# Kernel optimization log

Hardware: AMD Instinct MI355X
Metric: run time of the kernel (lower is better)

The kernel has to match this reference:

```python
import jax, jax.numpy as jnp
import numpy as np

LOG2PI = float(np.log(2.0 * np.pi))


def setup_inputs() -> dict:
    key = jax.random.key(0)
    ks = jax.random.split(key, 5)
    B, T, XD, C = 128, 2050, 6, 64
    return {
        "x": jax.random.normal(ks[0], (B, T, XD), jnp.float32),
        "observation_means": jax.random.uniform(ks[1], (C, XD), dtype=jnp.float32),
        "observation_stddevs": jax.random.uniform(ks[2], (C, XD), dtype=jnp.float32),
        "log_A": jax.random.normal(ks[3], (C, C), jnp.float32),
        "log_pi": jax.random.normal(ks[4], (C,), jnp.float32),
    }


def _emission_logprob(x, means, stds):
    # Normal(means[:, :4], relu(stds[:, :4]) + 0.1).log_prob(x[:, :, :4]) summed over feat dim
    mu = means[:, :4]                       # (C,4)
    sigma = jax.nn.relu(stds[:, :4]) + 0.1  # (C,4)
    z = (x[:, :, None, :4] - mu) / sigma    # (B,T,C,4)
    return jnp.sum(-0.5 * z * z - jnp.log(sigma) - 0.5 * LOG2PI, axis=-1)  # (B,T,C)


def _forward_scalers(logp, log_A, log_pi):
    # scaled HMM forward pass; returns per-step log normalizers (T,B)
    a0 = logp[:, 0] + log_pi
    s0 = jax.nn.logsumexp(a0, axis=-1)
    a0n = a0 - s0[:, None]

    def step(a_prev, lp_t):
        a = lp_t + jax.nn.logsumexp(a_prev[:, :, None] + log_A[None], axis=1)
        s = jax.nn.logsumexp(a, axis=-1)
        return a - s[:, None], s

    _, s_rest = jax.lax.scan(step, a0n, jnp.swapaxes(logp[:, 1:], 0, 1))
    return jnp.concatenate([s0[None], s_rest], axis=0)  # (T,B)


def _viterbi(logp, log_A, log_pi):
    d0 = logp[:, 0] + log_pi  # (B,C)

    def step(d_prev, lp_t):
        scores = d_prev[:, :, None] + log_A[None]  # (B,C_prev,C_cur)
        psi_t = jnp.argmax(scores, axis=1)
        d = jnp.max(scores, axis=1) + lp_t
        return d, psi_t

    d_last, psi = jax.lax.scan(step, d0, jnp.swapaxes(logp[:, 1:], 0, 1))  # psi: (T-1,B,C)
    c_last = jnp.argmax(d_last, axis=-1)  # (B,)

    def back(c_next, psi_t):
        c_t = jnp.take_along_axis(psi_t, c_next[:, None], axis=1)[:, 0]
        return c_t, c_t

    _, cs = jax.lax.scan(back, c_last, psi, reverse=True)  # (T-1,B)
    c = jnp.concatenate([cs, c_last[None]], axis=0)  # (T,B)
    return jnp.swapaxes(c, 0, 1)  # (B,T)


def reference(x, observation_means, observation_stddevs, log_A, log_pi):
    logA = jax.nn.log_softmax(log_A, axis=1)
    logpi = jax.nn.log_softmax(log_pi, axis=0)
    logp = _emission_logprob(x, observation_means, observation_stddevs)  # (B,T,C)
    scalers = _forward_scalers(logp, logA, logpi)                         # (T,B)
    logp_x = jnp.sum(scalers, axis=0)                                     # (B,)
    c_est = _viterbi(logp, logA, logpi)                                   # (B,T) int
    return logp_x, c_est
```

## Files before the change

kernel.cpp:

```cpp
#include <hip/hip_runtime.h>

#define T_LEN 2050
#define B_SZ 128
#define NCHUNK 33
#define HL2PI 0.91893853320467274178f

__device__ __forceinline__ float waveMax(float v) {
#pragma unroll
    for (int off = 32; off >= 1; off >>= 1)
        v = fmaxf(v, __shfl_xor(v, off, 64));
    return v;
}
__device__ __forceinline__ float waveSum(float v) {
#pragma unroll
    for (int off = 32; off >= 1; off >>= 1)
        v += __shfl_xor(v, off, 64);
    return v;
}
__device__ __forceinline__ void waveArgmax(float& v, int& idx) {
#pragma unroll
    for (int off = 32; off >= 1; off >>= 1) {
        float ov = __shfl_xor(v, off, 64);
        int   oi = __shfl_xor(idx, off, 64);
        if (ov > v || (ov == v && oi < idx)) { v = ov; idx = oi; }
    }
}
__device__ __forceinline__ void cfence() { asm volatile("" ::: "memory"); }

__device__ __forceinline__ float dppSumAll(float v) {
#define SSTEP(ctrl) { int t_ = __builtin_amdgcn_update_dpp(0, __float_as_int(v), ctrl, 0xf, 0xf, true); \
                      v = v + __int_as_float(t_); }
    SSTEP(0x111) SSTEP(0x112) SSTEP(0x114) SSTEP(0x118) SSTEP(0x142) SSTEP(0x143)
#undef SSTEP
    return __int_as_float(__builtin_amdgcn_readlane(__float_as_int(v), 63));
}
__device__ __forceinline__ float dppMaxAll(float v) {
#define MSTEP(ctrl) { int t_ = __builtin_amdgcn_update_dpp(__float_as_int(v), __float_as_int(v), ctrl, 0xf, 0xf, false); \
                      v = fmaxf(v, __int_as_float(t_)); }
    MSTEP(0x111) MSTEP(0x112) MSTEP(0x114) MSTEP(0x118) MSTEP(0x142) MSTEP(0x143)
#undef MSTEP
    return __int_as_float(__builtin_amdgcn_readlane(__float_as_int(v), 63));
}

extern "C" __global__ __launch_bounds__(64, 1)
void hmm_prep(const float* __restrict__ logA_in,
              const float* __restrict__ logpi_in,
              float* __restrict__ lAg,
              float* __restrict__ lpig)
{
    __shared__ float la[64 * 65];
    __shared__ float rowlse[64];
    const int j = threadIdx.x;
#pragma unroll
    for (int k = 0; k < 64; ++k)
        la[k * 65 + j] = logA_in[k * 64 + j];
    cfence();
    {
        float m = -1e30f;
#pragma unroll
        for (int k = 0; k < 64; ++k) m = fmaxf(m, la[j * 65 + k]);
        float s = 0.f;
#pragma unroll
        for (int k = 0; k < 64; ++k) s += expf(la[j * 65 + k] - m);
        rowlse[j] = m + logf(s);
    }
    cfence();
    {
        float v = logpi_in[j];
        float m = waveMax(v);
        float s = waveSum(expf(v - m));
        lpig[j] = v - (m + logf(s));
    }
    float4* o = (float4*)lAg;
#pragma unroll
    for (int k = 0; k < 16; ++k) {
        float4 v;
        v.x = la[(4 * k + 0) * 65 + j] - rowlse[4 * k + 0];
        v.y = la[(4 * k + 1) * 65 + j] - rowlse[4 * k + 1];
        v.z = la[(4 * k + 2) * 65 + j] - rowlse[4 * k + 2];
        v.w = la[(4 * k + 3) * 65 + j] - rowlse[4 * k + 3];
        o[j * 16 + k] = v;
    }
}

extern "C" __global__ __launch_bounds__(256)
void hmm_emis(const float* __restrict__ x,
              const float* __restrict__ means,
              const float* __restrict__ stds,
              float* __restrict__ buf,
              float* __restrict__ m_pre)
{
    const int wid = blockIdx.x * 4 + (threadIdx.x >> 6);
    const int j = threadIdx.x & 63;
    const int t = wid >> 7;
    const int b = wid & 127;

    const float* xt = x + ((size_t)b * T_LEN + t) * 6;
    float x0 = xt[0], x1 = xt[1], x2 = xt[2], x3 = xt[3];

    float mu0 = means[j * 6 + 0], mu1 = means[j * 6 + 1];
    float mu2 = means[j * 6 + 2], mu3 = means[j * 6 + 3];
    float sg0 = fmaxf(stds[j * 6 + 0], 0.f) + 0.1f;
    float sg1 = fmaxf(stds[j * 6 + 1], 0.f) + 0.1f;
    float sg2 = fmaxf(stds[j * 6 + 2], 0.f) + 0.1f;
    float sg3 = fmaxf(stds[j * 6 + 3], 0.f) + 0.1f;
    float ls0 = logf(sg0), ls1 = logf(sg1), ls2 = logf(sg2), ls3 = logf(sg3);

    float z0 = (x0 - mu0) / sg0, z1 = (x1 - mu1) / sg1;
    float z2 = (x2 - mu2) / sg2, z3 = (x3 - mu3) / sg3;
    float e0 = ((-0.5f * z0) * z0 - ls0) - HL2PI;
    float e1 = ((-0.5f * z1) * z1 - ls1) - HL2PI;
    float e2 = ((-0.5f * z2) * z2 - ls2) - HL2PI;
    float e3 = ((-0.5f * z3) * z3 - ls3) - HL2PI;
    float lp = ((e0 + e1) + e2) + e3;

    buf[((size_t)b * T_LEN + t) * 64 + j] = lp;
    float mm = waveMax(lp);
    if (j == 0) m_pre[(size_t)b * T_LEN + t] = mm;
}

extern "C" __global__ __launch_bounds__(64, 1)
void hmm_main(const float* __restrict__ x,
              const float* __restrict__ means,
              const float* __restrict__ stds,
              const float* __restrict__ lAg,
              const float* __restrict__ lpig,
              float* __restrict__ out,
              float* __restrict__ buf,
              const float* __restrict__ m_pre,
              int* __restrict__ c_last)
{
    __shared__ __align__(16) float xs[12304];
    __shared__ __align__(16) float pbuf[64];

    const int j   = threadIdx.x;
    const int bid = blockIdx.x;
    const bool is_fwd = (bid < B_SZ);
    const int b = is_fwd ? bid : bid - B_SZ;

    float lpi = lpig[j];
    const float4* pv = (const float4*)pbuf;

    if (is_fwd) {
        {
            const float4* xg4 = (const float4*)(x + (size_t)b * T_LEN * 6);
            float4* xs4 = (float4*)xs;
            for (int i = j; i < 3075; i += 64) xs4[i] = xg4[i];
        }
        float mu0 = means[j * 6 + 0], mu1 = means[j * 6 + 1];
        float mu2 = means[j * 6 + 2], mu3 = means[j * 6 + 3];
        float sg0 = fmaxf(stds[j * 6 + 0], 0.f) + 0.1f;
        float sg1 = fmaxf(stds[j * 6 + 1], 0.f) + 0.1f;
        float sg2 = fmaxf(stds[j * 6 + 2], 0.f) + 0.1f;
        float sg3 = fmaxf(stds[j * 6 + 3], 0.f) + 0.1f;
        float ls0 = logf(sg0), ls1 = logf(sg1), ls2 = logf(sg2), ls3 = logf(sg3);
        float i0 = 1.f / sg0, i1 = 1.f / sg1, i2 = 1.f / sg2, i3 = 1.f / sg3;
        float cst = -(ls0 + ls1 + ls2 + ls3) - 4.f * HL2PI;

        float Ac[64];
        {
            const float4* g = (const float4*)lAg;
#pragma unroll
            for (int k = 0; k < 16; ++k) {
                float4 v = g[j * 16 + k];
                Ac[4 * k + 0] = __expf(v.x); Ac[4 * k + 1] = __expf(v.y);
                Ac[4 * k + 2] = __expf(v.z); Ac[4 * k + 3] = __expf(v.w);
            }
        }
        cfence();

        float z0 = (xs[0] - mu0) * i0, z1 = (xs[1] - mu1) * i1;
        float z2 = (xs[2] - mu2) * i2, z3 = (xs[3] - mu3) * i3;
        float a0 = (cst - 0.5f * (z0 * z0 + z1 * z1 + z2 * z2 + z3 * z3)) + lpi;
        float m0a = dppMaxAll(a0);
        float u = __expf(a0 - m0a);
        float s0 = dppSumAll(u);
        double acc = (double)(m0a + __logf(s0));
        u *= (1.0f / s0);
        pbuf[j] = u;
        float4 rr[16];
#pragma unroll
        for (int k = 0; k < 16; ++k) rr[k] = pv[k];

        const float* mp = m_pre + (size_t)b * T_LEN;
        float g0 = mp[1], g1 = mp[2], g2 = mp[3], g3 = mp[4];

#pragma unroll 1
        for (int t = 1; t < T_LEN; ++t) {
            float mm_c = g0; g0 = g1; g1 = g2; g2 = g3;
            int tp = t + 4; if (tp > T_LEN - 1) tp = T_LEN - 1;
            g3 = mp[tp];

            int o = t * 6;
            float y0 = xs[o], y1 = xs[o + 1], y2 = xs[o + 2], y3 = xs[o + 3];
            float w0 = (y0 - mu0) * i0, w1 = (y1 - mu1) * i1;
            float w2 = (y2 - mu2) * i2, w3 = (y3 - mu3) * i3;
            float lp = cst - 0.5f * (w0 * w0 + w1 * w1 + w2 * w2 + w3 * w3);
            float e_c = __expf(lp - mm_c);

            float q0 = 0.f, q1 = 0.f, q2 = 0.f, q3 = 0.f;
#pragma unroll
            for (int k = 0; k < 16; ++k) {
                float4 pp = rr[k];
                q0 = fmaf(pp.x, Ac[4 * k + 0], q0);
                q1 = fmaf(pp.y, Ac[4 * k + 1], q1);
                q2 = fmaf(pp.z, Ac[4 * k + 2], q2);
                q3 = fmaf(pp.w, Ac[4 * k + 3], q3);
            }
            u = ((q0 + q1) + (q2 + q3)) * e_c;
            acc += (double)mm_c;
            if ((t & 3) == 0) {
                float ss = dppSumAll(u);
                acc += (double)__logf(ss);
                u *= (1.0f / ss);
            }

            pbuf[j] = u;
#pragma unroll
            for (int k = 0; k < 16; ++k) rr[k] = pv[k];
        }
        float sf = dppSumAll(u);
        acc += (double)__logf(sf);
        if (j == 0) out[b] = (float)acc;
    } else {
        float lA[64];
        {
            const float4* g = (const float4*)lAg;
#pragma unroll
            for (int k = 0; k < 16; ++k) {
                float4 v = g[j * 16 + k];
                lA[4 * k + 0] = v.x; lA[4 * k + 1] = v.y;
                lA[4 * k + 2] = v.z; lA[4 * k + 3] = v.w;
            }
        }
        float* bb = buf + (size_t)b * T_LEN * 64 + j;

        float dn = bb[0] + lpi;
        float l0 = bb[64], l1 = bb[128], l2 = bb[192], l3 = bb[256];
        bb[0] = dn;
        pbuf[j] = dn;
        float4 rr[16];
#pragma unroll
        for (int k = 0; k < 16; ++k) rr[k] = pv[k];

#pragma unroll 1
        for (int t = 1; t < T_LEN; ++t) {
            float lp_c = l0; l0 = l1; l1 = l2; l2 = l3;
            int tp = t + 4; if (tp > T_LEN - 1) tp = T_LEN - 1;
            l3 = bb[(size_t)tp * 64];

            float m0 = -3.4e38f, m1 = -3.4e38f, m2 = -3.4e38f, m3 = -3.4e38f;
#pragma unroll
            for (int k = 0; k < 16; ++k) {
                float4 dd = rr[k];
                m0 = fmaxf(m0, dd.x + lA[4 * k + 0]);
                m1 = fmaxf(m1, dd.y + lA[4 * k + 1]);
                m2 = fmaxf(m2, dd.z + lA[4 * k + 2]);
                m3 = fmaxf(m3, dd.w + lA[4 * k + 3]);
            }
            dn = fmaxf(fmaxf(m0, m1), fmaxf(m2, m3)) + lp_c;

            bb[(size_t)t * 64] = dn;
            pbuf[j] = dn;
#pragma unroll
            for (int k = 0; k < 16; ++k) rr[k] = pv[k];
        }

        float vv = dn; int idx = j;
        waveArgmax(vv, idx);
        if (j == 0) c_last[b] = idx;
    }
}

extern "C" __global__ __launch_bounds__(256)
void hmm_psi(const float* __restrict__ buf,
             const float* __restrict__ lAg,
             unsigned char* __restrict__ psi)
{
    __shared__ __align__(16) float sd[4][64];
    const int warp = threadIdx.x >> 6;
    const int j = threadIdx.x & 63;
    const int wid = blockIdx.x * 4 + warp;

    float lA[64];
    {
        const float4* g = (const float4*)lAg;
#pragma unroll
        for (int k = 0; k < 16; ++k) {
            float4 v = g[j * 16 + k];
            lA[4 * k + 0] = v.x; lA[4 * k + 1] = v.y;
            lA[4 * k + 2] = v.z; lA[4 * k + 3] = v.w;
        }
    }
    const float4* dv = (const float4*)sd[warp];
    const int NP = 2049 * B_SZ;

    for (int p = wid; p < NP; p += 8192) {
        const int t = (p >> 7) + 1;
        const int b = p & 127;
        float dval = buf[((size_t)b * T_LEN + (t - 1)) * 64 + j];
        sd[warp][j] = dval;

        float bv0 = -3.4e38f, bv1 = -3.4e38f, bv2 = -3.4e38f, bv3 = -3.4e38f;
        int bi0 = 0, bi1 = 1, bi2 = 2, bi3 = 3;
#pragma unroll
        for (int k = 0; k < 16; ++k) {
            float4 dd = dv[k];
            float v0 = dd.x + lA[4 * k + 0];
            float v1 = dd.y + lA[4 * k + 1];
            float v2 = dd.z + lA[4 * k + 2];
            float v3 = dd.w + lA[4 * k + 3];
            if (v0 > bv0) { bv0 = v0; bi0 = 4 * k + 0; }
            if (v1 > bv1) { bv1 = v1; bi1 = 4 * k + 1; }
            if (v2 > bv2) { bv2 = v2; bi2 = 4 * k + 2; }
            if (v3 > bv3) { bv3 = v3; bi3 = 4 * k + 3; }
        }
        float best = bv0; int bidx = bi0;
        if (bv1 > best || (bv1 == best && bi1 < bidx)) { best = bv1; bidx = bi1; }
        if (bv2 > best || (bv2 == best && bi2 < bidx)) { best = bv2; bidx = bi2; }
        if (bv3 > best || (bv3 == best && bi3 < bidx)) { best = bv3; bidx = bi3; }

        psi[((size_t)t * B_SZ + b) * 64 + j] = (unsigned char)bidx;
    }
}

extern "C" __global__ __launch_bounds__(256)
void hmm_compose(const unsigned char* __restrict__ psi,
                 unsigned char* __restrict__ mt)
{
    const int w = blockIdx.x * 4 + (threadIdx.x >> 6);
    const int j = threadIdx.x & 63;
    const int g = w % NCHUNK;
    const int b = w / NCHUNK;
    const int e = (g < NCHUNK - 1) ? g * 64 + 64 : (T_LEN - 1);
    int M = j;
    for (int t = e; t >= g * 64 + 1; --t)
        M = psi[((size_t)t * B_SZ + b) * 64 + M];
    mt[((size_t)g * B_SZ + b) * 64 + j] = (unsigned char)M;
}

extern "C" __global__ __launch_bounds__(64, 1)
void hmm_fill(const unsigned char* __restrict__ psi,
              const unsigned char* __restrict__ mt,
              const int* __restrict__ c_last,
              float* __restrict__ out)
{
    __shared__ int sb[NCHUNK];
    const int b = blockIdx.x;
    const int g = threadIdx.x;
    const int cl = c_last[b];
    if (g == 0) {
        int cur = cl;
        for (int q = NCHUNK - 1; q >= 0; --q) {
            cur = mt[((size_t)q * B_SZ + b) * 64 + cur];
            sb[q] = cur;
        }
    }
    cfence();
    float* oc = out + B_SZ + (size_t)b * T_LEN;
    if (g == NCHUNK) {
        oc[T_LEN - 1] = (float)cl;
    } else if (g < NCHUNK) {
        const int e = (g < NCHUNK - 1) ? g * 64 + 64 : (T_LEN - 1);
        int s = (g < NCHUNK - 1) ? sb[g + 1] : cl;
        for (int t = e; t >= g * 64 + 1; --t) {
            s = psi[((size_t)t * B_SZ + b) * 64 + s];
            oc[t - 1] = (float)s;
        }
    }
}

extern "C" void kernel_launch(void* const* d_in, const int* in_sizes, int n_in,
                              void* d_out, int out_size, void* d_ws, size_t ws_size,
                              hipStream_t stream)
{
    const float* x      = (const float*)d_in[0];
    const float* means  = (const float*)d_in[1];
    const float* stds   = (const float*)d_in[2];
    const float* logA   = (const float*)d_in[3];
    const float* logpi  = (const float*)d_in[4];
    float* out = (float*)d_out;

    char* base = (char*)d_ws;
    float*         buf   = (float*)base;
    unsigned char* psi   = (unsigned char*)(base + 67174400);
    float*         m_pre = (float*)(base + 67174400);
    unsigned char* mt    = (unsigned char*)(base + 83968000);
    int*           cl    = (int*)(base + 84238336);
    float*         lAg   = (float*)(base + 84238848);
    float*         lpig  = (float*)(base + 84255232);

    hipLaunchKernelGGL(hmm_prep, dim3(1), dim3(64), 0, stream, logA, logpi, lAg, lpig);
    hipLaunchKernelGGL(hmm_emis, dim3((T_LEN * B_SZ) / 4), dim3(256), 0, stream,
                       x, means, stds, buf, m_pre);
    hipLaunchKernelGGL(hmm_main, dim3(2 * B_SZ), dim3(64), 0, stream,
                       x, means, stds, lAg, lpig, out, buf, m_pre, cl);
    hipLaunchKernelGGL(hmm_psi, dim3(2048), dim3(256), 0, stream, buf, lAg, psi);
    hipLaunchKernelGGL(hmm_compose, dim3((NCHUNK * B_SZ) / 4), dim3(256), 0, stream, psi, mt);
    hipLaunchKernelGGL(hmm_fill, dim3(B_SZ), dim3(64), 0, stream, psi, mt, cl, out);
}
```

Baseline: 1.055 ms.

## Split HMM recurrence inner product across two wavefronts per batch

The sequential forward and Viterbi recurrence in hmm_main now uses two wavefronts per block. Each wavefront reduces over half of the 64 previous states, and the partial sums or maxima are combined through shared memory with a block barrier every time step. This halves the per-step FMA and max chain and the register footprint per lane. In exchange it adds a __syncthreads and an LDS round trip to every one of roughly 2050 serial steps, which may cost more than the arithmetic it saves.

```diff
diff --git a/kernel.cpp b/kernel.cpp
--- a/kernel.cpp
+++ b/kernel.cpp
@@ -119,7 +119,7 @@
     if (j == 0) m_pre[(size_t)b * T_LEN + t] = mm;
 }
 
-extern "C" __global__ __launch_bounds__(64, 1)
+extern "C" __global__ __launch_bounds__(128, 1)
 void hmm_main(const float* __restrict__ x,
               const float* __restrict__ means,
               const float* __restrict__ stds,
@@ -131,21 +131,25 @@
               int* __restrict__ c_last)
 {
     __shared__ __align__(16) float xs[12304];
-    __shared__ __align__(16) float pbuf[64];
-
-    const int j   = threadIdx.x;
+    __shared__ __align__(16) float uperm[2][64];
+    __shared__ float pexch[2][2][64];
+
+    const int tid = threadIdx.x;
+    const int w   = tid >> 6;
+    const int j   = tid & 63;
     const int bid = blockIdx.x;
     const bool is_fwd = (bid < B_SZ);
     const int b = is_fwd ? bid : bid - B_SZ;
+    const int slot = (j & 3) * 16 + (j >> 2);
 
     float lpi = lpig[j];
-    const float4* pv = (const float4*)pbuf;
+    const float4* pv = (const float4*)(&uperm[w][32 * w]);
 
     if (is_fwd) {
         {
             const float4* xg4 = (const float4*)(x + (size_t)b * T_LEN * 6);
             float4* xs4 = (float4*)xs;
-            for (int i = j; i < 3075; i += 64) xs4[i] = xg4[i];
+            for (int i = tid; i < 3075; i += 128) xs4[i] = xg4[i];
         }
         float mu0 = means[j * 6 + 0], mu1 = means[j * 6 + 1];
         float mu2 = means[j * 6 + 2], mu3 = means[j * 6 + 3];
@@ -157,17 +161,24 @@
         float i0 = 1.f / sg0, i1 = 1.f / sg1, i2 = 1.f / sg2, i3 = 1.f / sg3;
         float cst = -(ls0 + ls1 + ls2 + ls3) - 4.f * HL2PI;
 
-        float Ac[64];
+        float Aa[16], Ab[16];
         {
             const float4* g = (const float4*)lAg;
-#pragma unroll
-            for (int k = 0; k < 16; ++k) {
-                float4 v = g[j * 16 + k];
-                Ac[4 * k + 0] = __expf(v.x); Ac[4 * k + 1] = __expf(v.y);
-                Ac[4 * k + 2] = __expf(v.z); Ac[4 * k + 3] = __expf(v.w);
+            if (w == 0) {
+#pragma unroll
+                for (int k = 0; k < 16; ++k) {
+                    float4 v = g[j * 16 + k];
+                    Aa[k] = __expf(v.x); Ab[k] = __expf(v.y);
+                }
+            } else {
+#pragma unroll
+                for (int k = 0; k < 16; ++k) {
+                    float4 v = g[j * 16 + k];
+                    Aa[k] = __expf(v.z); Ab[k] = __expf(v.w);
+                }
             }
         }
-        cfence();
+        __syncthreads();
 
         float z0 = (xs[0] - mu0) * i0, z1 = (xs[1] - mu1) * i1;
         float z2 = (xs[2] - mu2) * i2, z3 = (xs[3] - mu3) * i3;
@@ -177,10 +188,10 @@
         float s0 = dppSumAll(u);
         double acc = (double)(m0a + __logf(s0));
         u *= (1.0f / s0);
-        pbuf[j] = u;
-        float4 rr[16];
-#pragma unroll
-        for (int k = 0; k < 16; ++k) rr[k] = pv[k];
+        uperm[w][slot] = u;
+        float4 rrA[8];
+#pragma unroll
+        for (int k = 0; k < 8; ++k) rrA[k] = pv[k];
 
         const float* mp = m_pre + (size_t)b * T_LEN;
         float g0 = mp[1], g1 = mp[2], g2 = mp[3], g3 = mp[4];
@@ -198,16 +209,23 @@
             float lp = cst - 0.5f * (w0 * w0 + w1 * w1 + w2 * w2 + w3 * w3);
             float e_c = __expf(lp - mm_c);
 
-            float q0 = 0.f, q1 = 0.f, q2 = 0.f, q3 = 0.f;
-#pragma unroll
-            for (int k = 0; k < 16; ++k) {
-                float4 pp = rr[k];
-                q0 = fmaf(pp.x, Ac[4 * k + 0], q0);
-                q1 = fmaf(pp.y, Ac[4 * k + 1], q1);
-                q2 = fmaf(pp.z, Ac[4 * k + 2], q2);
-                q3 = fmaf(pp.w, Ac[4 * k + 3], q3);
+            float qa = 0.f, qb = 0.f;
+#pragma unroll
+            for (int c = 0; c < 4; ++c) {
+                float4 va = rrA[c], vb = rrA[4 + c];
+                qa = fmaf(va.x, Aa[4 * c + 0], qa);
+                qa = fmaf(va.y, Aa[4 * c + 1], qa);
+                qa = fmaf(va.z, Aa[4 * c + 2], qa);
+                qa = fmaf(va.w, Aa[4 * c + 3], qa);
+                qb = fmaf(vb.x, Ab[4 * c + 0], qb);
+                qb = fmaf(vb.y, Ab[4 * c + 1], qb);
+                qb = fmaf(vb.z, Ab[4 * c + 2], qb);
+                qb = fmaf(vb.w, Ab[4 * c + 3], qb);
             }
-            u = ((q0 + q1) + (q2 + q3)) * e_c;
+            float part = qa + qb;
+            pexch[t & 1][w][j] = part;
+            __syncthreads();
+            u = (part + pexch[t & 1][w ^ 1][j]) * e_c;
             acc += (double)mm_c;
             if ((t & 3) == 0) {
                 float ss = dppSumAll(u);
@@ -215,33 +233,41 @@
                 u *= (1.0f / ss);
             }
 
-            pbuf[j] = u;
-#pragma unroll
-            for (int k = 0; k < 16; ++k) rr[k] = pv[k];
+            uperm[w][slot] = u;
+#pragma unroll
+            for (int k = 0; k < 8; ++k) rrA[k] = pv[k];
         }
         float sf = dppSumAll(u);
         acc += (double)__logf(sf);
-        if (j == 0) out[b] = (float)acc;
+        if (w == 0 && j == 0) out[b] = (float)acc;
     } else {
-        float lA[64];
+        float Aa[16], Ab[16];
         {
             const float4* g = (const float4*)lAg;
-#pragma unroll
-            for (int k = 0; k < 16; ++k) {
-                float4 v = g[j * 16 + k];
-                lA[4 * k + 0] = v.x; lA[4 * k + 1] = v.y;
-                lA[4 * k + 2] = v.z; lA[4 * k + 3] = v.w;
+            if (w == 0) {
+#pragma unroll
+                for (int k = 0; k < 16; ++k) {
+                    float4 v = g[j * 16 + k];
+                    Aa[k] = v.x; Ab[k] = v.y;
+                }
+            } else {
+#pragma unroll
+                for (int k = 0; k < 16; ++k) {
+                    float4 v = g[j * 16 + k];
+                    Aa[k] = v.z; Ab[k] = v.w;
+                }
             }
         }
         float* bb = buf + (size_t)b * T_LEN * 64 + j;
 
         float dn = bb[0] + lpi;
         float l0 = bb[64], l1 = bb[128], l2 = bb[192], l3 = bb[256];
-        bb[0] = dn;
-        pbuf[j] = dn;
-        float4 rr[16];
-#pragma unroll
-        for (int k = 0; k < 16; ++k) rr[k] = pv[k];
+        __syncthreads();
+        if (w == 0) bb[0] = dn;
+        uperm[w][slot] = dn;
+        float4 rrA[8];
+#pragma unroll
+        for (int k = 0; k < 8; ++k) rrA[k] = pv[k];
 
 #pragma unroll 1
         for (int t = 1; t < T_LEN; ++t) {
@@ -249,26 +275,33 @@
             int tp = t + 4; if (tp > T_LEN - 1) tp = T_LEN - 1;
             l3 = bb[(size_t)tp * 64];
 
-            float m0 = -3.4e38f, m1 = -3.4e38f, m2 = -3.4e38f, m3 = -3.4e38f;
-#pragma unroll
-            for (int k = 0; k < 16; ++k) {
-                float4 dd = rr[k];
-                m0 = fmaxf(m0, dd.x + lA[4 * k + 0]);
-                m1 = fmaxf(m1, dd.y + lA[4 * k + 1]);
-                m2 = fmaxf(m2, dd.z + lA[4 * k + 2]);
-                m3 = fmaxf(m3, dd.w + lA[4 * k + 3]);
+            float ma = -3.4e38f, mb = -3.4e38f;
+#pragma unroll
+            for (int c = 0; c < 4; ++c) {
+                float4 va = rrA[c], vb = rrA[4 + c];
+                float a0_ = va.x + Aa[4 * c + 0], a1_ = va.y + Aa[4 * c + 1];
+                float a2_ = va.z + Aa[4 * c + 2], a3_ = va.w + Aa[4 * c + 3];
+                ma = fmaxf(fmaxf(ma, a0_), a1_);
+                ma = fmaxf(fmaxf(ma, a2_), a3_);
+                float b0_ = vb.x + Ab[4 * c + 0], b1_ = vb.y + Ab[4 * c + 1];
+                float b2_ = vb.z + Ab[4 * c + 2], b3_ = vb.w + Ab[4 * c + 3];
+                mb = fmaxf(fmaxf(mb, b0_), b1_);
+                mb = fmaxf(fmaxf(mb, b2_), b3_);
             }
-            dn = fmaxf(fmaxf(m0, m1), fmaxf(m2, m3)) + lp_c;
-
-            bb[(size_t)t * 64] = dn;
-            pbuf[j] = dn;
-#pragma unroll
-            for (int k = 0; k < 16; ++k) rr[k] = pv[k];
+            float part = fmaxf(ma, mb);
+            pexch[t & 1][w][j] = part;
+            __syncthreads();
+            dn = fmaxf(part, pexch[t & 1][w ^ 1][j]) + lp_c;
+
+            if (w == 0) bb[(size_t)t * 64] = dn;
+            uperm[w][slot] = dn;
+#pragma unroll
+            for (int k = 0; k < 8; ++k) rrA[k] = pv[k];
         }
 
         float vv = dn; int idx = j;
         waveArgmax(vv, idx);
-        if (j == 0) c_last[b] = idx;
+        if (w == 0 && j == 0) c_last[b] = idx;
     }
 }
 
@@ -393,7 +426,7 @@
     hipLaunchKernelGGL(hmm_prep, dim3(1), dim3(64), 0, stream, logA, logpi, lAg, lpig);
     hipLaunchKernelGGL(hmm_emis, dim3((T_LEN * B_SZ) / 4), dim3(256), 0, stream,
                        x, means, stds, buf, m_pre);
-    hipLaunchKernelGGL(hmm_main, dim3(2 * B_SZ), dim3(64), 0, stream,
+    hipLaunchKernelGGL(hmm_main, dim3(2 * B_SZ), dim3(128), 0, stream,
                        x, means, stds, lAg, lpig, out, buf, m_pre, cl);
     hipLaunchKernelGGL(hmm_psi, dim3(2048), dim3(256), 0, stream, buf, lAg, psi);
     hipLaunchKernelGGL(hmm_compose, dim3((NCHUNK * B_SZ) / 4), dim3(256), 0, stream, psi, mt);
```

New measurement: 1.005 ms. 4.7% less time.
